# Kernel tuning notes

Measured on AMD Instinct MI355X. Metric: run time of the kernel, lower is better.

Reference implementation:

```python
import jax, jax.numpy as jnp
import numpy as np

NUM_HEADS = 16
HEAD_DIM = 64  # hidden = 1024


def setup_inputs() -> dict:
    key = jax.random.key(0)
    k1, k2, k3 = jax.random.split(key, 3)
    B, S, Hd = 4, 4096, NUM_HEADS * HEAD_DIM
    x = jax.random.normal(k1, (B, S, Hd), dtype=jnp.float32)
    # xavier-uniform-ish scaling for the dense kernels
    Wqkv = jax.random.normal(k2, (Hd, 3 * Hd), dtype=jnp.float32) * (2.0 / (Hd + 3 * Hd)) ** 0.5
    bqkv = jnp.zeros((3 * Hd,), dtype=jnp.float32)
    Wout = jax.random.normal(k3, (Hd, Hd), dtype=jnp.float32) * (1.0 / Hd) ** 0.5
    bout = jnp.zeros((Hd,), dtype=jnp.float32)
    return {"x": x, "Wqkv": Wqkv, "bqkv": bqkv, "Wout": Wout, "bout": bout}


def reference(x, Wqkv, bqkv, Wout, bout):
    B, S, _ = x.shape
    H, D = NUM_HEADS, HEAD_DIM
    qkv = jnp.einsum('bsc,cf->bsf', x, Wqkv) + bqkv  # [B,S,3*H*D]
    q, k, v = jnp.split(qkv, 3, axis=-1)
    # source transposes to [B,H,S,D] before calling flax dot_product_attention_weights,
    # which interprets dims as [..., q_len=H, num_heads=S, depth=D]  (shape bug, kept faithfully)
    q = q.reshape(B, S, H, D).transpose(0, 2, 1, 3)  # [B,H,S,D]
    k = k.reshape(B, S, H, D).transpose(0, 2, 1, 3)
    v = v.reshape(B, S, H, D).transpose(0, 2, 1, 3)
    scale = D ** -0.5
    # flax: einsum('...qhd,...khd->...hqk') -> weights [B, S, H, H]
    logits = jnp.einsum('bqhd,bkhd->bhqk', q * scale, k)
    attn = jax.nn.softmax(logits, axis=-1)  # softmax over key-head axis
    # source: einsum('bhqk,bkhd->bqhd', weights, v) -> [B, H, S, D]
    out = jnp.einsum('bhqk,bkhd->bqhd', attn, v)
    out = out.transpose(0, 2, 1, 3).reshape(B, S, H * D)  # [B,S,hidden]
    return jnp.einsum('bsc,cf->bsf', out, Wout) + bout
```

## Files before the change

kernel.cpp:

```cpp
#include <hip/hip_runtime.h>
#include <hip/hip_bf16.h>

using bf16 = __hip_bfloat16;
typedef __bf16 bf16x8_t __attribute__((ext_vector_type(8)));
typedef float f32x4_t __attribute__((ext_vector_type(4)));

__device__ __forceinline__ void gl16(bf16* l, const bf16* g) {
  __builtin_amdgcn_global_load_lds(
      (const __attribute__((address_space(1))) unsigned int*)g,
      (__attribute__((address_space(3))) unsigned int*)l, 16, 0, 0);
}

#define BARRIER() do { asm volatile("" ::: "memory"); __builtin_amdgcn_s_barrier(); asm volatile("" ::: "memory"); } while (0)
#define WAITVM(N) asm volatile("s_waitcnt vmcnt(" #N ")" ::: "memory")
#define SCHED0() __builtin_amdgcn_sched_barrier(0)

__global__ __launch_bounds__(256) void prep_fused(const float* __restrict__ x,
                                                  const float* __restrict__ Wqkv,
                                                  const float* __restrict__ Wout,
                                                  bf16* __restrict__ xb,
                                                  bf16* __restrict__ w1t,
                                                  bf16* __restrict__ w2t) {
  __shared__ float t[32][33];
  const int bid = blockIdx.x;
  if (bid < 16384) {
    int i = bid * 256 + threadIdx.x;
    float4 v = ((const float4*)x)[i];
    union { ushort4 u; bf16 b[4]; } o;
    o.b[0] = __float2bfloat16(v.x);
    o.b[1] = __float2bfloat16(v.y);
    o.b[2] = __float2bfloat16(v.z);
    o.b[3] = __float2bfloat16(v.w);
    ((ushort4*)xb)[i] = o.u;
    return;
  }
  const float* in; bf16* out; int R, C, gx, gy;
  if (bid < 16384 + 3072) {
    int idx = bid - 16384; in = Wqkv; out = w1t; R = 1024; C = 3072;
    gx = idx % 96; gy = idx / 96;
  } else {
    int idx = bid - 16384 - 3072; in = Wout; out = w2t; R = 1024; C = 1024;
    gx = idx & 31; gy = idx >> 5;
  }
  int bx = gx * 32, by = gy * 32;
  int tx = threadIdx.x & 31, ty = threadIdx.x >> 5;
#pragma unroll
  for (int r = 0; r < 32; r += 8)
    t[ty + r][tx] = in[(size_t)(by + ty + r) * C + bx + tx];
  __syncthreads();
#pragma unroll
  for (int r = 0; r < 32; r += 8)
    out[(size_t)(bx + ty + r) * R + by + tx] = __float2bfloat16(t[tx][ty + r]);
}


__device__ __forceinline__ void readA(const bf16* lb, int half, int wr, int lr, int lg, int exr,
                                      bf16x8_t (&af)[4][2]) {
  const bf16* ab = lb + half * 8192;
#pragma unroll
  for (int mi = 0; mi < 4; ++mi) {
    int R = wr * 64 + mi * 16 + lr;
    af[mi][0] = *(const bf16x8_t*)(ab + R * 64 + ((lg * 8) ^ exr));
    af[mi][1] = *(const bf16x8_t*)(ab + R * 64 + ((32 + lg * 8) ^ exr));
  }
}
__device__ __forceinline__ void readB(const bf16* lb, int half, int wc, int lr, int lg, int exr,
                                      bf16x8_t (&bfr)[2][2]) {
  const bf16* bb = lb + (2 + half) * 8192;
#pragma unroll
  for (int ni = 0; ni < 2; ++ni) {
    int R = wc * 32 + ni * 16 + lr;
    bfr[ni][0] = *(const bf16x8_t*)(bb + R * 64 + ((lg * 8) ^ exr));
    bfr[ni][1] = *(const bf16x8_t*)(bb + R * 64 + ((32 + lg * 8) ^ exr));
  }
}

template <int MH, int NH>
__device__ __forceinline__ void mfma16(bf16x8_t (&af)[4][2], bf16x8_t (&bfr)[2][2],
                                       f32x4_t (&acc)[8][4]) {
  __builtin_amdgcn_s_setprio(1);
#pragma unroll
  for (int mi = 0; mi < 4; ++mi)
#pragma unroll
    for (int ni = 0; ni < 2; ++ni) {
      f32x4_t& a = acc[MH * 4 + mi][NH * 2 + ni];
      a = __builtin_amdgcn_mfma_f32_16x16x32_bf16(af[mi][0], bfr[ni][0], a, 0, 0, 0);
      a = __builtin_amdgcn_mfma_f32_16x16x32_bf16(af[mi][1], bfr[ni][1], a, 0, 0, 0);
    }
  __builtin_amdgcn_s_setprio(0);
}

template <int OUT_BF16, int NWGX>
__global__ __launch_bounds__(512, 2) void gemm256p(const bf16* __restrict__ A,
                                                   const bf16* __restrict__ Bt,
                                                   const float* __restrict__ bias,
                                                   void* __restrict__ Cv) {
  constexpr int K = 1024;
  constexpr int N = NWGX * 256;
  constexpr int TT = NWGX / 4;
  constexpr int G = TT * 16;
  constexpr int CPX = NWGX * 8;

  __shared__ __align__(16) bf16 lds[65536];
  const int tid = threadIdx.x;
  const int bx = blockIdx.x;

  const int wid = tid >> 6, lane = tid & 63;
  const int wr = wid >> 2, wc = wid & 3;
  const int lr = lane & 15, lg = lane >> 4;
  const int exr = (lr & 7) << 3;

  const int srow = tid >> 3;
  const int colg = ((((tid & 7) * 16) ^ ((srow & 7) << 4)) >> 1);
  const int browc0 = (srow >> 5) * 64 + (srow & 31);

  auto tileMN = [&](int tt, int& m0, int& n0) {
    int orig = bx + (tt << 8);
    int swz = (orig & 7) * CPX + (orig >> 3);
    m0 = (swz / NWGX) * 256;
    n0 = (swz % NWGX) * 256;
  };

  auto stageA = [&](int g, int h) {
    if (g >= G) return;
    int m0, n0; tileMN(g >> 4, m0, n0);
    const bf16* g0 = A + (size_t)(m0 + h * 64 + srow) * K + (g & 15) * 64 + colg;
    bf16* l = lds + (g & 1) * 32768 + h * 8192 + tid * 8;
    gl16(l, g0); gl16(l + 4096, g0 + (size_t)128 * K);
  };
  auto stageB = [&](int g, int h) {
    if (g >= G) return;
    int m0, n0; tileMN(g >> 4, m0, n0);
    const bf16* g0 = Bt + (size_t)(n0 + browc0 + h * 32) * K + (g & 15) * 64 + colg;
    bf16* l = lds + (g & 1) * 32768 + (2 + h) * 8192 + tid * 8;
    gl16(l, g0); gl16(l + 4096, g0 + (size_t)128 * K);
  };

  f32x4_t acc[8][4] = {};
  bf16x8_t af1[4][2], af2[4][2], b0[2][2], b1[2][2];

  stageA(0, 0); stageB(0, 0); stageA(0, 1); stageB(0, 1);
  stageA(1, 0); stageB(1, 0);
  WAITVM(4);
  BARRIER();
  readA(lds, 0, wr, lr, lg, exr, af1);
  readB(lds, 0, wc, lr, lg, exr, b0);

  for (int g = 0; g < G; ++g) {
    const bf16* cb = lds + (g & 1) * 32768;
    const bf16* nb = lds + ((g & 1) ^ 1) * 32768;

    stageA(g + 1, 1);
    BARRIER();
    readB(cb, 1, wc, lr, lg, exr, b1);
    SCHED0();
    mfma16<0, 0>(af1, b0, acc);

    stageB(g + 1, 1);
    BARRIER();
    readA(cb, 1, wr, lr, lg, exr, af2);
    SCHED0();
    mfma16<0, 1>(af1, b1, acc);

    stageA(g + 2, 0);
    BARRIER();
    mfma16<1, 0>(af2, b0, acc);

    stageB(g + 2, 0);
    if (g < G - 2) { WAITVM(4); } else { WAITVM(0); }
    BARRIER();
    if (g < G - 1) {
      readA(nb, 0, wr, lr, lg, exr, af1);
      readB(nb, 0, wc, lr, lg, exr, b0);
      SCHED0();
    }
    mfma16<1, 1>(af2, b1, acc);

    if ((g & 15) == 15) {
      BARRIER();
      int m0, n0; tileMN(g >> 4, m0, n0);
      float bv[4];
#pragma unroll
      for (int n = 0; n < 4; ++n) bv[n] = bias[n0 + wc * 64 + n * 16 + lr];
#pragma unroll
      for (int m = 0; m < 8; ++m) {
        int row = m0 + wr * 128 + m * 16 + lg * 4;
#pragma unroll
        for (int j = 0; j < 4; ++j) {
#pragma unroll
          for (int n = 0; n < 4; ++n) {
            int col = n0 + wc * 64 + n * 16 + lr;
            float v = acc[m][n][j] + bv[n];
            if (OUT_BF16)
              ((bf16*)Cv)[(size_t)(row + j) * N + col] = __float2bfloat16(v);
            else
              ((float*)Cv)[(size_t)(row + j) * N + col] = v;
            acc[m][n][j] = 0.f;
          }
        }
      }
    }
  }
}

#define PSTR 48
__global__ __launch_bounds__(256) void attn_tok(const bf16* __restrict__ qkv,
                                                bf16* __restrict__ out) {
  __shared__ __align__(16) bf16 vs[4][1024];
  __shared__ __align__(16) bf16 ps[4][16 * PSTR];
  const int w = threadIdx.x >> 6, l = threadIdx.x & 63;
  const int t = blockIdx.x * 4 + w;
  const int lr = l & 15, lg = l >> 4;
  const bf16* base = qkv + (size_t)t * 3072;

  bf16x8_t v0 = *(const bf16x8_t*)(base + 2048 + l * 16);
  bf16x8_t v1 = *(const bf16x8_t*)(base + 2048 + l * 16 + 8);
  *(bf16x8_t*)(&vs[w][l * 16]) = v0;
  *(bf16x8_t*)(&vs[w][l * 16 + 8]) = v1;

  *(unsigned long long*)(&ps[w][(l >> 2) * PSTR + 16 + (l & 3) * 4]) = 0ULL;

  const bf16* qp = base + lr * 64 + lg * 8;
  const bf16* kp = base + 1024 + lr * 64 + lg * 8;
  bf16x8_t qa0 = *(const bf16x8_t*)qp;
  bf16x8_t ka0 = *(const bf16x8_t*)kp;
  bf16x8_t qa1 = *(const bf16x8_t*)(qp + 32);
  bf16x8_t ka1 = *(const bf16x8_t*)(kp + 32);
  f32x4_t s = {};
  s = __builtin_amdgcn_mfma_f32_16x16x32_bf16(qa0, ka0, s, 0, 0, 0);
  s = __builtin_amdgcn_mfma_f32_16x16x32_bf16(qa1, ka1, s, 0, 0, 0);

#pragma unroll
  for (int j = 0; j < 4; ++j) {
    float x = s[j] * 0.125f;
    float mx = x;
#pragma unroll
    for (int off = 8; off; off >>= 1) mx = fmaxf(mx, __shfl_xor(mx, off, 16));
    float e = __expf(x - mx);
    float sum = e;
#pragma unroll
    for (int off = 8; off; off >>= 1) sum += __shfl_xor(sum, off, 16);
    ps[w][(lg * 4 + j) * PSTR + lr] = __float2bfloat16(e / sum);
  }

  bf16x8_t pf = *(const bf16x8_t*)(&ps[w][lr * PSTR + lg * 8]);
  bf16x8_t vf[4] = {};
  if (l < 32) {
#pragma unroll
    for (int c = 0; c < 4; ++c)
#pragma unroll
      for (int j = 0; j < 8; ++j)
        vf[c][j] = (__bf16)vs[w][(lg * 8 + j) * 64 + c * 16 + lr];
  }
  f32x4_t o[4] = {};
#pragma unroll
  for (int c = 0; c < 4; ++c)
    o[c] = __builtin_amdgcn_mfma_f32_16x16x32_bf16(pf, vf[c], o[c], 0, 0, 0);

  bf16* ob = out + (size_t)t * 1024;
#pragma unroll
  for (int c = 0; c < 4; ++c)
#pragma unroll
    for (int j = 0; j < 4; ++j)
      ob[(lg * 4 + j) * 64 + c * 16 + lr] = __float2bfloat16(o[c][j]);
}

extern "C" void kernel_launch(void* const* d_in, const int* in_sizes, int n_in,
                              void* d_out, int out_size, void* d_ws, size_t ws_size,
                              hipStream_t stream) {
  const float* x    = (const float*)d_in[0];
  const float* Wqkv = (const float*)d_in[1];
  const float* bqkv = (const float*)d_in[2];
  const float* Wout = (const float*)d_in[3];
  const float* bout = (const float*)d_in[4];
  float* y = (float*)d_out;

  const int T = 16384, HD = 1024, N1 = 3072;

  char* ws = (char*)d_ws;
  size_t off = 0;
  bf16* xb  = (bf16*)(ws + off); off += (size_t)T * HD * 2;
  bf16* w1t = (bf16*)(ws + off); off += (size_t)N1 * HD * 2;
  bf16* w2t = (bf16*)(ws + off); off += (size_t)HD * HD * 2;
  bf16* qkv = (bf16*)(ws + off); off += (size_t)T * N1 * 2;
  if (ws_size < off) return;
  bf16* ao = xb;

  prep_fused<<<16384 + 3072 + 1024, 256, 0, stream>>>(x, Wqkv, Wout, xb, w1t, w2t);
  gemm256p<1, 12><<<256, 512, 0, stream>>>(xb, w1t, bqkv, qkv);
  attn_tok<<<T / 4, 256, 0, stream>>>(qkv, ao);
  gemm256p<0, 4><<<256, 512, 0, stream>>>(ao, w2t, bout, y);
}
```

Measured before the change: 199.2 us.

## Switch GEMM mainloop to BK=32 with four-stage LDS ring buffer

The 256x256 bf16 GEMM now uses a K-step of 32 instead of 64 and a 4-deep LDS ring, prefetching three steps ahead instead of one. LDS layout and swizzle move to 32-element rows with XOR on the row's low two bits, and the wait counts are retuned for the deeper pipeline. The goal is to hide global-load latency better. In exchange it doubles the number of iterations and barriers per tile and halves MFMA work per barrier, so synchronisation overhead rises.

```diff
diff --git a/kernel.cpp b/kernel.cpp
--- a/kernel.cpp
+++ b/kernel.cpp
@@ -54,39 +54,34 @@
 }
 
 
-__device__ __forceinline__ void readA(const bf16* lb, int half, int wr, int lr, int lg, int exr,
-                                      bf16x8_t (&af)[4][2]) {
-  const bf16* ab = lb + half * 8192;
+__device__ __forceinline__ void readA(const bf16* buf, int MH, int wr, int lr, int lg,
+                                      bf16x8_t (&af)[4]) {
 #pragma unroll
   for (int mi = 0; mi < 4; ++mi) {
-    int R = wr * 64 + mi * 16 + lr;
-    af[mi][0] = *(const bf16x8_t*)(ab + R * 64 + ((lg * 8) ^ exr));
-    af[mi][1] = *(const bf16x8_t*)(ab + R * 64 + ((32 + lg * 8) ^ exr));
-  }
-}
-__device__ __forceinline__ void readB(const bf16* lb, int half, int wc, int lr, int lg, int exr,
-                                      bf16x8_t (&bfr)[2][2]) {
-  const bf16* bb = lb + (2 + half) * 8192;
+    int R = wr * 128 + MH * 64 + mi * 16 + lr;
+    af[mi] = *(const bf16x8_t*)(buf + R * 32 + ((lg ^ (R & 3)) << 3));
+  }
+}
+__device__ __forceinline__ void readB(const bf16* buf, int NH, int wc, int lr, int lg,
+                                      bf16x8_t (&bfr)[2]) {
+  const bf16* bb = buf + 8192;
 #pragma unroll
   for (int ni = 0; ni < 2; ++ni) {
-    int R = wc * 32 + ni * 16 + lr;
-    bfr[ni][0] = *(const bf16x8_t*)(bb + R * 64 + ((lg * 8) ^ exr));
-    bfr[ni][1] = *(const bf16x8_t*)(bb + R * 64 + ((32 + lg * 8) ^ exr));
+    int R = wc * 64 + NH * 32 + ni * 16 + lr;
+    bfr[ni] = *(const bf16x8_t*)(bb + R * 32 + ((lg ^ (R & 3)) << 3));
   }
 }
 
 template <int MH, int NH>
-__device__ __forceinline__ void mfma16(bf16x8_t (&af)[4][2], bf16x8_t (&bfr)[2][2],
-                                       f32x4_t (&acc)[8][4]) {
+__device__ __forceinline__ void mfma8(bf16x8_t (&af)[4], bf16x8_t (&bfr)[2],
+                                      f32x4_t (&acc)[8][4]) {
   __builtin_amdgcn_s_setprio(1);
 #pragma unroll
   for (int mi = 0; mi < 4; ++mi)
 #pragma unroll
-    for (int ni = 0; ni < 2; ++ni) {
-      f32x4_t& a = acc[MH * 4 + mi][NH * 2 + ni];
-      a = __builtin_amdgcn_mfma_f32_16x16x32_bf16(af[mi][0], bfr[ni][0], a, 0, 0, 0);
-      a = __builtin_amdgcn_mfma_f32_16x16x32_bf16(af[mi][1], bfr[ni][1], a, 0, 0, 0);
-    }
+    for (int ni = 0; ni < 2; ++ni)
+      acc[MH * 4 + mi][NH * 2 + ni] = __builtin_amdgcn_mfma_f32_16x16x32_bf16(
+          af[mi], bfr[ni], acc[MH * 4 + mi][NH * 2 + ni], 0, 0, 0);
   __builtin_amdgcn_s_setprio(0);
 }
 
@@ -98,7 +93,7 @@
   constexpr int K = 1024;
   constexpr int N = NWGX * 256;
   constexpr int TT = NWGX / 4;
-  constexpr int G = TT * 16;
+  constexpr int G = TT * 32;
   constexpr int CPX = NWGX * 8;
 
   __shared__ __align__(16) bf16 lds[65536];
@@ -108,11 +103,9 @@
   const int wid = tid >> 6, lane = tid & 63;
   const int wr = wid >> 2, wc = wid & 3;
   const int lr = lane & 15, lg = lane >> 4;
-  const int exr = (lr & 7) << 3;
-
-  const int srow = tid >> 3;
-  const int colg = ((((tid & 7) * 16) ^ ((srow & 7) << 4)) >> 1);
-  const int browc0 = (srow >> 5) * 64 + (srow & 31);
+
+  const int srow = tid >> 2;
+  const int colg = (((tid & 3) ^ (srow & 3)) << 3);
 
   auto tileMN = [&](int tt, int& m0, int& n0) {
     int orig = bx + (tt << 8);
@@ -121,64 +114,63 @@
     n0 = (swz % NWGX) * 256;
   };
 
-  auto stageA = [&](int g, int h) {
+  auto stageA = [&](int g) {
     if (g >= G) return;
-    int m0, n0; tileMN(g >> 4, m0, n0);
-    const bf16* g0 = A + (size_t)(m0 + h * 64 + srow) * K + (g & 15) * 64 + colg;
-    bf16* l = lds + (g & 1) * 32768 + h * 8192 + tid * 8;
+    int m0, n0; tileMN(g >> 5, m0, n0);
+    const bf16* g0 = A + (size_t)(m0 + srow) * K + (g & 31) * 32 + colg;
+    bf16* l = lds + (g & 3) * 16384 + tid * 8;
     gl16(l, g0); gl16(l + 4096, g0 + (size_t)128 * K);
   };
-  auto stageB = [&](int g, int h) {
+  auto stageB = [&](int g) {
     if (g >= G) return;
-    int m0, n0; tileMN(g >> 4, m0, n0);
-    const bf16* g0 = Bt + (size_t)(n0 + browc0 + h * 32) * K + (g & 15) * 64 + colg;
-    bf16* l = lds + (g & 1) * 32768 + (2 + h) * 8192 + tid * 8;
+    int m0, n0; tileMN(g >> 5, m0, n0);
+    const bf16* g0 = Bt + (size_t)(n0 + srow) * K + (g & 31) * 32 + colg;
+    bf16* l = lds + (g & 3) * 16384 + 8192 + tid * 8;
     gl16(l, g0); gl16(l + 4096, g0 + (size_t)128 * K);
   };
 
   f32x4_t acc[8][4] = {};
-  bf16x8_t af1[4][2], af2[4][2], b0[2][2], b1[2][2];
-
-  stageA(0, 0); stageB(0, 0); stageA(0, 1); stageB(0, 1);
-  stageA(1, 0); stageB(1, 0);
-  WAITVM(4);
+  bf16x8_t af1[4], af2[4], b0[2], b1[2];
+
+  stageA(0); stageB(0); stageA(1); stageB(1); stageA(2); stageB(2);
+  WAITVM(8);
   BARRIER();
-  readA(lds, 0, wr, lr, lg, exr, af1);
-  readB(lds, 0, wc, lr, lg, exr, b0);
+  readA(lds, 0, wr, lr, lg, af1);
+  readB(lds, 0, wc, lr, lg, b0);
 
   for (int g = 0; g < G; ++g) {
-    const bf16* cb = lds + (g & 1) * 32768;
-    const bf16* nb = lds + ((g & 1) ^ 1) * 32768;
-
-    stageA(g + 1, 1);
-    BARRIER();
-    readB(cb, 1, wc, lr, lg, exr, b1);
+    const bf16* cb = lds + (g & 3) * 16384;
+    const bf16* nb = lds + ((g + 1) & 3) * 16384;
+
+    stageA(g + 3);
+    BARRIER();
+    readB(cb, 1, wc, lr, lg, b1);
     SCHED0();
-    mfma16<0, 0>(af1, b0, acc);
-
-    stageB(g + 1, 1);
-    BARRIER();
-    readA(cb, 1, wr, lr, lg, exr, af2);
+    mfma8<0, 0>(af1, b0, acc);
+
+    stageB(g + 3);
+    BARRIER();
+    readA(cb, 1, wr, lr, lg, af2);
     SCHED0();
-    mfma16<0, 1>(af1, b1, acc);
-
-    stageA(g + 2, 0);
-    BARRIER();
-    mfma16<1, 0>(af2, b0, acc);
-
-    stageB(g + 2, 0);
-    if (g < G - 2) { WAITVM(4); } else { WAITVM(0); }
+    mfma8<0, 1>(af1, b1, acc);
+
+    BARRIER();
+    mfma8<1, 0>(af2, b0, acc);
+
+    if (g + 3 < G)       { WAITVM(8); }
+    else if (g + 3 == G) { WAITVM(4); }
+    else if (g + 2 == G) { WAITVM(0); }
     BARRIER();
     if (g < G - 1) {
-      readA(nb, 0, wr, lr, lg, exr, af1);
-      readB(nb, 0, wc, lr, lg, exr, b0);
+      readA(nb, 0, wr, lr, lg, af1);
+      readB(nb, 0, wc, lr, lg, b0);
       SCHED0();
     }
-    mfma16<1, 1>(af2, b1, acc);
-
-    if ((g & 15) == 15) {
+    mfma8<1, 1>(af2, b1, acc);
+
+    if ((g & 31) == 31) {
       BARRIER();
-      int m0, n0; tileMN(g >> 4, m0, n0);
+      int m0, n0; tileMN(g >> 5, m0, n0);
       float bv[4];
 #pragma unroll
       for (int n = 0; n < 4; ++n) bv[n] = bias[n0 + wc * 64 + n * 16 + lr];
```

Result: slower. 203.5 us (+2.2%).

## Restructure GEMM main loop into barrier-separated ping-pong phases with explicit LDS waits

Applied to the files above, without the earlier changes.

Reorganizes the double-buffered GEMM main loop so each quarter-step first issues LDS fragment reads and the next global-to-LDS stage, then waits on lgkmcnt before its MFMA block, with barriers on both sides of every MFMA group. Fragment reads for the next tile are no longer prefetched across the loop boundary. The prologue and the vmcnt wait depths change to match the new staging order. This aims for a more regular, ping-pong style schedule across waves, at the cost of extra barriers and less register-level prefetching.

```diff
diff --git a/kernel.cpp b/kernel.cpp
--- a/kernel.cpp
+++ b/kernel.cpp
@@ -13,7 +13,7 @@
 
 #define BARRIER() do { asm volatile("" ::: "memory"); __builtin_amdgcn_s_barrier(); asm volatile("" ::: "memory"); } while (0)
 #define WAITVM(N) asm volatile("s_waitcnt vmcnt(" #N ")" ::: "memory")
-#define SCHED0() __builtin_amdgcn_sched_barrier(0)
+#define LGKM0() do { asm volatile("s_waitcnt lgkmcnt(0)" ::: "memory"); __builtin_amdgcn_sched_barrier(0); } while (0)
 
 __global__ __launch_bounds__(256) void prep_fused(const float* __restrict__ x,
                                                   const float* __restrict__ Wqkv,
@@ -137,47 +137,46 @@
   };
 
   f32x4_t acc[8][4] = {};
-  bf16x8_t af1[4][2], af2[4][2], b0[2][2], b1[2][2];
+  bf16x8_t a1[4][2], a2[4][2], b0[2][2], b1[2][2];
 
   stageA(0, 0); stageB(0, 0); stageA(0, 1); stageB(0, 1);
-  stageA(1, 0); stageB(1, 0);
-  WAITVM(4);
+  stageA(1, 0); stageB(1, 0); stageA(1, 1);
+  WAITVM(6);
   BARRIER();
-  readA(lds, 0, wr, lr, lg, exr, af1);
-  readB(lds, 0, wc, lr, lg, exr, b0);
 
   for (int g = 0; g < G; ++g) {
     const bf16* cb = lds + (g & 1) * 32768;
-    const bf16* nb = lds + ((g & 1) ^ 1) * 32768;
-
-    stageA(g + 1, 1);
-    BARRIER();
+
+    readA(cb, 0, wr, lr, lg, exr, a1);
+    readB(cb, 0, wc, lr, lg, exr, b0);
+    stageB(g + 1, 1);
+    BARRIER();
+    LGKM0();
+    mfma16<0, 0>(a1, b0, acc);
+    BARRIER();
+
     readB(cb, 1, wc, lr, lg, exr, b1);
-    SCHED0();
-    mfma16<0, 0>(af1, b0, acc);
-
-    stageB(g + 1, 1);
-    BARRIER();
-    readA(cb, 1, wr, lr, lg, exr, af2);
-    SCHED0();
-    mfma16<0, 1>(af1, b1, acc);
-
     stageA(g + 2, 0);
     BARRIER();
-    mfma16<1, 0>(af2, b0, acc);
-
+    LGKM0();
+    mfma16<0, 1>(a1, b1, acc);
+    BARRIER();
+
+    readA(cb, 1, wr, lr, lg, exr, a2);
     stageB(g + 2, 0);
-    if (g < G - 2) { WAITVM(4); } else { WAITVM(0); }
-    BARRIER();
-    if (g < G - 1) {
-      readA(nb, 0, wr, lr, lg, exr, af1);
-      readB(nb, 0, wc, lr, lg, exr, b0);
-      SCHED0();
-    }
-    mfma16<1, 1>(af2, b1, acc);
+    BARRIER();
+    LGKM0();
+    mfma16<1, 0>(a2, b0, acc);
+    BARRIER();
+
+    stageA(g + 2, 1);
+    if (g + 2 < G)       { WAITVM(6); }
+    else if (g + 2 == G) { WAITVM(0); }
+    BARRIER();
+    mfma16<1, 1>(a2, b1, acc);
+    BARRIER();
 
     if ((g & 15) == 15) {
-      BARRIER();
       int m0, n0; tileMN(g >> 4, m0, n0);
       float bv[4];
 #pragma unroll
```

Result: no change. 199.5 us (+0.1%).

## Replace persistent GEMM with one-tile-per-block kernel and precomputed LDS pointers

Applied to the files above, without the earlier changes.

The persistent GEMM that looped over several output tiles per block is replaced by a non-persistent kernel that launches one block per 256x256 tile (768 blocks for the QKV projection). The K loop is fully unrolled in pairs, and global and LDS addresses are precomputed, which removes per-iteration tile index math and branches. The intent is to cut address overhead and rely on the hardware scheduler for tile distribution. The cost is losing the cross-tile prefetch overlap and paying block launch and prologue per tile.

```diff
diff --git a/kernel.cpp b/kernel.cpp
--- a/kernel.cpp
+++ b/kernel.cpp
@@ -54,24 +54,20 @@
 }
 
 
-__device__ __forceinline__ void readA(const bf16* lb, int half, int wr, int lr, int lg, int exr,
-                                      bf16x8_t (&af)[4][2]) {
-  const bf16* ab = lb + half * 8192;
+template <int H, int P>
+__device__ __forceinline__ void readAx(const bf16* pA0, const bf16* pA1, bf16x8_t (&af)[4][2]) {
 #pragma unroll
   for (int mi = 0; mi < 4; ++mi) {
-    int R = wr * 64 + mi * 16 + lr;
-    af[mi][0] = *(const bf16x8_t*)(ab + R * 64 + ((lg * 8) ^ exr));
-    af[mi][1] = *(const bf16x8_t*)(ab + R * 64 + ((32 + lg * 8) ^ exr));
-  }
-}
-__device__ __forceinline__ void readB(const bf16* lb, int half, int wc, int lr, int lg, int exr,
-                                      bf16x8_t (&bfr)[2][2]) {
-  const bf16* bb = lb + (2 + half) * 8192;
+    af[mi][0] = *(const bf16x8_t*)(pA0 + mi * 1024 + H * 16384 + P * 8192);
+    af[mi][1] = *(const bf16x8_t*)(pA1 + mi * 1024 + H * 16384 + P * 8192);
+  }
+}
+template <int H, int P>
+__device__ __forceinline__ void readBx(const bf16* pB0, const bf16* pB1, bf16x8_t (&bfr)[2][2]) {
 #pragma unroll
   for (int ni = 0; ni < 2; ++ni) {
-    int R = wc * 32 + ni * 16 + lr;
-    bfr[ni][0] = *(const bf16x8_t*)(bb + R * 64 + ((lg * 8) ^ exr));
-    bfr[ni][1] = *(const bf16x8_t*)(bb + R * 64 + ((32 + lg * 8) ^ exr));
+    bfr[ni][0] = *(const bf16x8_t*)(pB0 + ni * 1024 + H * 16384 + P * 8192);
+    bfr[ni][1] = *(const bf16x8_t*)(pB1 + ni * 1024 + H * 16384 + P * 8192);
   }
 }
 
@@ -90,114 +86,155 @@
   __builtin_amdgcn_s_setprio(0);
 }
 
-template <int OUT_BF16, int NWGX>
-__global__ __launch_bounds__(512, 2) void gemm256p(const bf16* __restrict__ A,
+template <int OUT_BF16, int NG, int NWGX>
+__global__ __launch_bounds__(512, 2) void gemm256s(const bf16* __restrict__ A,
                                                    const bf16* __restrict__ Bt,
                                                    const float* __restrict__ bias,
                                                    void* __restrict__ Cv) {
   constexpr int K = 1024;
   constexpr int N = NWGX * 256;
-  constexpr int TT = NWGX / 4;
-  constexpr int G = TT * 16;
-  constexpr int CPX = NWGX * 8;
-
+  constexpr int Q = NG / 8;
   __shared__ __align__(16) bf16 lds[65536];
-  const int tid = threadIdx.x;
-  const int bx = blockIdx.x;
+  const int tid = threadIdx.x, bx = blockIdx.x;
+  const int swz = (bx & 7) * Q + (bx >> 3);
+  const int m0 = (swz / NWGX) * 256, n0 = (swz % NWGX) * 256;
 
   const int wid = tid >> 6, lane = tid & 63;
   const int wr = wid >> 2, wc = wid & 3;
   const int lr = lane & 15, lg = lane >> 4;
   const int exr = (lr & 7) << 3;
-
   const int srow = tid >> 3;
   const int colg = ((((tid & 7) * 16) ^ ((srow & 7) << 4)) >> 1);
   const int browc0 = (srow >> 5) * 64 + (srow & 31);
 
-  auto tileMN = [&](int tt, int& m0, int& n0) {
-    int orig = bx + (tt << 8);
-    int swz = (orig & 7) * CPX + (orig >> 3);
-    m0 = (swz / NWGX) * 256;
-    n0 = (swz % NWGX) * 256;
+  const bf16* gA0l = A + (size_t)(m0 + srow) * K + colg;
+  const bf16* gA0h = gA0l + (size_t)128 * K;
+  const bf16* gA1l = A + (size_t)(m0 + 64 + srow) * K + colg;
+  const bf16* gA1h = gA1l + (size_t)128 * K;
+  const bf16* gB0l = Bt + (size_t)(n0 + browc0) * K + colg;
+  const bf16* gB0h = gB0l + (size_t)128 * K;
+  const bf16* gB1l = Bt + (size_t)(n0 + browc0 + 32) * K + colg;
+  const bf16* gB1h = gB1l + (size_t)128 * K;
+  bf16* ldsSt = lds + tid * 8;
+
+  const bf16* pA0 = lds + (wr * 64 + lr) * 64 + ((lg * 8) ^ exr);
+  const bf16* pA1 = lds + (wr * 64 + lr) * 64 + ((32 + lg * 8) ^ exr);
+  const bf16* pB0 = lds + 32768 + (wc * 32 + lr) * 64 + ((lg * 8) ^ exr);
+  const bf16* pB1 = lds + 32768 + (wc * 32 + lr) * 64 + ((32 + lg * 8) ^ exr);
+
+  auto stA = [&](const bf16* lo, const bf16* hi, int loff) {
+    gl16(ldsSt + loff, lo); gl16(ldsSt + loff + 4096, hi);
   };
-
-  auto stageA = [&](int g, int h) {
-    if (g >= G) return;
-    int m0, n0; tileMN(g >> 4, m0, n0);
-    const bf16* g0 = A + (size_t)(m0 + h * 64 + srow) * K + (g & 15) * 64 + colg;
-    bf16* l = lds + (g & 1) * 32768 + h * 8192 + tid * 8;
-    gl16(l, g0); gl16(l + 4096, g0 + (size_t)128 * K);
-  };
-  auto stageB = [&](int g, int h) {
-    if (g >= G) return;
-    int m0, n0; tileMN(g >> 4, m0, n0);
-    const bf16* g0 = Bt + (size_t)(n0 + browc0 + h * 32) * K + (g & 15) * 64 + colg;
-    bf16* l = lds + (g & 1) * 32768 + (2 + h) * 8192 + tid * 8;
-    gl16(l, g0); gl16(l + 4096, g0 + (size_t)128 * K);
+  auto stB = [&](const bf16* lo, const bf16* hi, int loff) {
+    gl16(ldsSt + 32768 + loff, lo); gl16(ldsSt + 32768 + loff + 4096, hi);
   };
 
   f32x4_t acc[8][4] = {};
   bf16x8_t af1[4][2], af2[4][2], b0[2][2], b1[2][2];
 
-  stageA(0, 0); stageB(0, 0); stageA(0, 1); stageB(0, 1);
-  stageA(1, 0); stageB(1, 0);
+  stA(gA0l, gA0h, 0);                 stB(gB0l, gB0h, 0);
+  stA(gA1l, gA1h, 16384);             stB(gB1l, gB1h, 16384);
+  stA(gA0l + 64, gA0h + 64, 8192);    stB(gB0l + 64, gB0h + 64, 8192);
   WAITVM(4);
   BARRIER();
-  readA(lds, 0, wr, lr, lg, exr, af1);
-  readB(lds, 0, wc, lr, lg, exr, b0);
-
-  for (int g = 0; g < G; ++g) {
-    const bf16* cb = lds + (g & 1) * 32768;
-    const bf16* nb = lds + ((g & 1) ^ 1) * 32768;
-
-    stageA(g + 1, 1);
-    BARRIER();
-    readB(cb, 1, wc, lr, lg, exr, b1);
-    SCHED0();
+  readAx<0, 0>(pA0, pA1, af1);
+  readBx<0, 0>(pB0, pB1, b0);
+
+  for (int gs = 0; gs < 14; gs += 2) {
+    {
+      stA(gA1l + (gs + 1) * 64, gA1h + (gs + 1) * 64, 16384 + 8192);
+      BARRIER();
+      readBx<1, 0>(pB0, pB1, b1); SCHED0();
+      mfma16<0, 0>(af1, b0, acc);
+
+      stB(gB1l + (gs + 1) * 64, gB1h + (gs + 1) * 64, 16384 + 8192);
+      BARRIER();
+      readAx<1, 0>(pA0, pA1, af2); SCHED0();
+      mfma16<0, 1>(af1, b1, acc);
+
+      stA(gA0l + (gs + 2) * 64, gA0h + (gs + 2) * 64, 0);
+      BARRIER();
+      mfma16<1, 0>(af2, b0, acc);
+
+      stB(gB0l + (gs + 2) * 64, gB0h + (gs + 2) * 64, 0);
+      WAITVM(4);
+      BARRIER();
+      readAx<0, 1>(pA0, pA1, af1);
+      readBx<0, 1>(pB0, pB1, b0); SCHED0();
+      mfma16<1, 1>(af2, b1, acc);
+    }
+    {
+      stA(gA1l + (gs + 2) * 64, gA1h + (gs + 2) * 64, 16384);
+      BARRIER();
+      readBx<1, 1>(pB0, pB1, b1); SCHED0();
+      mfma16<0, 0>(af1, b0, acc);
+
+      stB(gB1l + (gs + 2) * 64, gB1h + (gs + 2) * 64, 16384);
+      BARRIER();
+      readAx<1, 1>(pA0, pA1, af2); SCHED0();
+      mfma16<0, 1>(af1, b1, acc);
+
+      stA(gA0l + (gs + 3) * 64, gA0h + (gs + 3) * 64, 8192);
+      BARRIER();
+      mfma16<1, 0>(af2, b0, acc);
+
+      stB(gB0l + (gs + 3) * 64, gB0h + (gs + 3) * 64, 8192);
+      WAITVM(4);
+      BARRIER();
+      readAx<0, 0>(pA0, pA1, af1);
+      readBx<0, 0>(pB0, pB1, b0); SCHED0();
+      mfma16<1, 1>(af2, b1, acc);
+    }
+  }
+  {
+    stA(gA1l + 15 * 64, gA1h + 15 * 64, 16384 + 8192);
+    BARRIER();
+    readBx<1, 0>(pB0, pB1, b1); SCHED0();
     mfma16<0, 0>(af1, b0, acc);
 
-    stageB(g + 1, 1);
-    BARRIER();
-    readA(cb, 1, wr, lr, lg, exr, af2);
-    SCHED0();
+    stB(gB1l + 15 * 64, gB1h + 15 * 64, 16384 + 8192);
+    BARRIER();
+    readAx<1, 0>(pA0, pA1, af2); SCHED0();
     mfma16<0, 1>(af1, b1, acc);
 
-    stageA(g + 2, 0);
     BARRIER();
     mfma16<1, 0>(af2, b0, acc);
 
-    stageB(g + 2, 0);
-    if (g < G - 2) { WAITVM(4); } else { WAITVM(0); }
-    BARRIER();
-    if (g < G - 1) {
-      readA(nb, 0, wr, lr, lg, exr, af1);
-      readB(nb, 0, wc, lr, lg, exr, b0);
-      SCHED0();
-    }
+    WAITVM(0);
+    BARRIER();
+    readAx<0, 1>(pA0, pA1, af1);
+    readBx<0, 1>(pB0, pB1, b0); SCHED0();
     mfma16<1, 1>(af2, b1, acc);
-
-    if ((g & 15) == 15) {
-      BARRIER();
-      int m0, n0; tileMN(g >> 4, m0, n0);
-      float bv[4];
-#pragma unroll
-      for (int n = 0; n < 4; ++n) bv[n] = bias[n0 + wc * 64 + n * 16 + lr];
-#pragma unroll
-      for (int m = 0; m < 8; ++m) {
-        int row = m0 + wr * 128 + m * 16 + lg * 4;
-#pragma unroll
-        for (int j = 0; j < 4; ++j) {
-#pragma unroll
-          for (int n = 0; n < 4; ++n) {
-            int col = n0 + wc * 64 + n * 16 + lr;
-            float v = acc[m][n][j] + bv[n];
-            if (OUT_BF16)
-              ((bf16*)Cv)[(size_t)(row + j) * N + col] = __float2bfloat16(v);
-            else
-              ((float*)Cv)[(size_t)(row + j) * N + col] = v;
-            acc[m][n][j] = 0.f;
-          }
-        }
+  }
+  {
+    BARRIER();
+    readBx<1, 1>(pB0, pB1, b1); SCHED0();
+    mfma16<0, 0>(af1, b0, acc);
+    BARRIER();
+    readAx<1, 1>(pA0, pA1, af2); SCHED0();
+    mfma16<0, 1>(af1, b1, acc);
+    BARRIER();
+    mfma16<1, 0>(af2, b0, acc);
+    BARRIER();
+    mfma16<1, 1>(af2, b1, acc);
+  }
+
+  float bv[4];
+#pragma unroll
+  for (int n = 0; n < 4; ++n) bv[n] = bias[n0 + wc * 64 + n * 16 + lr];
+#pragma unroll
+  for (int m = 0; m < 8; ++m) {
+    int row = m0 + wr * 128 + m * 16 + lg * 4;
+#pragma unroll
+    for (int j = 0; j < 4; ++j) {
+#pragma unroll
+      for (int n = 0; n < 4; ++n) {
+        int col = n0 + wc * 64 + n * 16 + lr;
+        float v = acc[m][n][j] + bv[n];
+        if (OUT_BF16)
+          ((bf16*)Cv)[(size_t)(row + j) * N + col] = __float2bfloat16(v);
+        else
+          ((float*)Cv)[(size_t)(row + j) * N + col] = v;
       }
     }
   }
@@ -287,7 +324,7 @@
   bf16* ao = xb;
 
   prep_fused<<<16384 + 3072 + 1024, 256, 0, stream>>>(x, Wqkv, Wout, xb, w1t, w2t);
-  gemm256p<1, 12><<<256, 512, 0, stream>>>(xb, w1t, bqkv, qkv);
+  gemm256s<1, 768, 12><<<768, 512, 0, stream>>>(xb, w1t, bqkv, qkv);
   attn_tok<<<T / 4, 256, 0, stream>>>(qkv, ao);
-  gemm256p<0, 4><<<256, 512, 0, stream>>>(ao, w2t, bout, y);
-}
+  gemm256s<0, 256, 4><<<256, 512, 0, stream>>>(ao, w2t, bout, y);
+}
```

Measured after the change: 201.4 us. Within noise of the previous version (+1.1%).
